# Performance work log

Measured on AMD Instinct MI355X. Metric: run time of the kernel, lower is better.

## Reference

```python
import jax, jax.numpy as jnp
import numpy as np

T, B, D = 1024, 16, 1024
BETA_INIT = 2.0


def _beta_gemm(beta_param, t):
    # beta = sigmoid(raw param); lower-triangular matrix M[i, j] = beta**(i-j) for j <= i
    beta = jax.nn.sigmoid(beta_param)
    i = jnp.arange(t)[:, None]
    j = jnp.arange(t)[None, :]
    expo = i - j                      # [T, T]
    mask = expo >= 0
    # clamp exponent in masked-out region to avoid inf from negative powers
    mat = beta ** jnp.where(mask, expo, 0).astype(beta.dtype)
    return jnp.where(mask, mat, jnp.zeros((), beta.dtype))


def setup_inputs() -> dict:
    key = jax.random.key(0)
    k1, _ = jax.random.split(key)
    x_seq = jax.random.normal(k1, (T, B, D), dtype=jnp.float32)
    beta_param = jnp.asarray(BETA_INIT, dtype=jnp.float32)
    return {"x_seq": x_seq, "beta_param": beta_param}


def reference(x_seq, beta_param):
    t = x_seq.shape[0]
    beta_gemm = _beta_gemm(beta_param, t)            # [T, T] lower-tri decay
    flat = x_seq.reshape(t, -1)                       # [T, B*D]
    y = beta_gemm @ flat                              # addmm with zero bias
    return y.reshape(x_seq.shape)
```

## Files before the change

kernel.cpp:

```cpp
#include <hip/hip_runtime.h>
#include <math.h>

#define T_DIM 1024
#define C_DIM 16384
#define WAVES 16
#define BLOCK_T (WAVES * 64)
#define L_CHUNK (T_DIM / WAVES)

__global__ __launch_bounds__(BLOCK_T, 4)
void pli_scan_kernel(const float* __restrict__ x,
                     const float* __restrict__ beta_p,
                     float* __restrict__ out) {
    const int lane = threadIdx.x & 63;
    const int w    = threadIdx.x >> 6;
    const int col  = (blockIdx.x << 6) + lane;

    const float beta = 1.0f / (1.0f + expf(-beta_p[0]));

    const size_t base = (size_t)(w * L_CHUNK) * C_DIM + col;
    const float* xp = x + base;

    float v[L_CHUNK];
#pragma unroll
    for (int t = 0; t < L_CHUNK; ++t) {
        v[t] = xp[(size_t)t * C_DIM];
    }

    float run = 0.0f;
#pragma unroll
    for (int t = 0; t < L_CHUNK; ++t) {
        run = fmaf(run, beta, v[t]);
        v[t] = run;
    }

    __shared__ float carry[WAVES][64];
    carry[w][lane] = run;
    __syncthreads();

    float bL = beta;
#pragma unroll
    for (int i = 0; i < 6; ++i) bL *= bL;

    float Y = 0.0f;
    for (int u = 0; u < w; ++u) {
        Y = fmaf(Y, bL, carry[u][lane]);
    }

    float m = beta * Y;
    float* op = out + base;
#pragma unroll
    for (int t = 0; t < L_CHUNK; ++t) {
        op[(size_t)t * C_DIM] = v[t] + m;
        m *= beta;
    }
}

extern "C" void kernel_launch(void* const* d_in, const int* in_sizes, int n_in,
                              void* d_out, int out_size, void* d_ws, size_t ws_size,
                              hipStream_t stream) {
    const float* x      = (const float*)d_in[0];
    const float* beta_p = (const float*)d_in[1];
    float* out          = (float*)d_out;

    dim3 grid(C_DIM / 64);
    dim3 block(BLOCK_T);
    hipLaunchKernelGGL(pli_scan_kernel, grid, block, 0, stream, x, beta_p, out);
}
```

Before: 110.4 us.

## Use cooperative grid-sync chunked scan with global carry workspace

Adds a cooperative kernel that splits time into 16 chunks across blocks instead of across waves within one block. Each block does a local scan, writes its chunk carry to a global workspace, syncs the whole grid, then adds the decayed prefix of earlier carries. The aim is wider rows per block for better coalescing and a different work layout. In exchange it adds a grid-wide barrier, global carry traffic and a dependence on cooperative launch support and workspace size. The old kernel remains as a fallback.

```diff
diff --git a/kernel.cpp b/kernel.cpp
--- a/kernel.cpp
+++ b/kernel.cpp
@@ -1,8 +1,67 @@
 #include <hip/hip_runtime.h>
+#include <hip/hip_cooperative_groups.h>
 #include <math.h>
 
 #define T_DIM 1024
 #define C_DIM 16384
+#define TGROUPS 16
+#define CGROUPS 16
+#define TC (T_DIM / TGROUPS)
+#define CC (C_DIM / CGROUPS)
+#define BLOCK_N 1024
+
+namespace cg = cooperative_groups;
+
+__global__ __launch_bounds__(BLOCK_N, 4)
+void pli_scan_coop(const float* __restrict__ x,
+                   const float* __restrict__ beta_p,
+                   float* __restrict__ out,
+                   float* __restrict__ carry) {
+    const int tg  = blockIdx.x >> 4;
+    const int cgi = blockIdx.x & 15;
+    const int col = (cgi << 10) + threadIdx.x;
+
+    const float beta = 1.0f / (1.0f + expf(-beta_p[0]));
+
+    const size_t base = (size_t)(tg * TC) * C_DIM + col;
+    const float* xp = x + base;
+
+    float v[TC];
+#pragma unroll
+    for (int r = 0; r < TC; ++r) {
+        v[r] = xp[(size_t)r * C_DIM];
+    }
+
+    float run = 0.0f;
+#pragma unroll
+    for (int r = 0; r < TC; ++r) {
+        run = fmaf(run, beta, v[r]);
+        v[r] = run;
+    }
+
+    carry[tg * C_DIM + col] = run;
+
+    __threadfence();
+    cg::this_grid().sync();
+
+    float bL = beta;
+#pragma unroll
+    for (int i = 0; i < 6; ++i) bL *= bL;
+
+    float Y = 0.0f;
+    for (int u = 0; u < tg; ++u) {
+        Y = fmaf(Y, bL, carry[u * C_DIM + col]);
+    }
+
+    float m = beta * Y;
+    float* op = out + base;
+#pragma unroll
+    for (int r = 0; r < TC; ++r) {
+        op[(size_t)r * C_DIM] = v[r] + m;
+        m *= beta;
+    }
+}
+
 #define WAVES 16
 #define BLOCK_T (WAVES * 64)
 #define L_CHUNK (T_DIM / WAVES)
@@ -22,19 +81,14 @@
 
     float v[L_CHUNK];
 #pragma unroll
-    for (int t = 0; t < L_CHUNK; ++t) {
-        v[t] = xp[(size_t)t * C_DIM];
-    }
+    for (int t = 0; t < L_CHUNK; ++t) v[t] = xp[(size_t)t * C_DIM];
 
     float run = 0.0f;
 #pragma unroll
-    for (int t = 0; t < L_CHUNK; ++t) {
-        run = fmaf(run, beta, v[t]);
-        v[t] = run;
-    }
+    for (int t = 0; t < L_CHUNK; ++t) { run = fmaf(run, beta, v[t]); v[t] = run; }
 
-    __shared__ float carry[WAVES][64];
-    carry[w][lane] = run;
+    __shared__ float carry_s[WAVES][64];
+    carry_s[w][lane] = run;
     __syncthreads();
 
     float bL = beta;
@@ -42,9 +96,7 @@
     for (int i = 0; i < 6; ++i) bL *= bL;
 
     float Y = 0.0f;
-    for (int u = 0; u < w; ++u) {
-        Y = fmaf(Y, bL, carry[u][lane]);
-    }
+    for (int u = 0; u < w; ++u) Y = fmaf(Y, bL, carry_s[u][lane]);
 
     float m = beta * Y;
     float* op = out + base;
@@ -62,7 +114,19 @@
     const float* beta_p = (const float*)d_in[1];
     float* out          = (float*)d_out;
 
-    dim3 grid(C_DIM / 64);
-    dim3 block(BLOCK_T);
-    hipLaunchKernelGGL(pli_scan_kernel, grid, block, 0, stream, x, beta_p, out);
+    const size_t carry_bytes = (size_t)TGROUPS * C_DIM * sizeof(float);
+
+    if (d_ws != nullptr && ws_size >= carry_bytes) {
+        float* carry = (float*)d_ws;
+        dim3 grid(TGROUPS * CGROUPS);
+        dim3 block(BLOCK_N);
+        void* args[] = { (void*)&x, (void*)&beta_p, (void*)&out, (void*)&carry };
+        hipLaunchCooperativeKernel((const void*)pli_scan_coop, grid, block,
+                                   args, 0, stream);
+    } else {
+        dim3 grid(C_DIM / 64);
+        dim3 block(BLOCK_T);
+        hipLaunchKernelGGL(pli_scan_kernel, grid, block, 0, stream,
+                           x, beta_p, out);
+    }
 }
```

Result: slower. 252.0 us (+128.3%).

## Split scan into carry and apply kernels with float4 loads across time groups

Applied to the files above, without the earlier changes.

Replaces the single-kernel chunked scan with two kernels: one that computes per-time-chunk carries into workspace, and one that folds the preceding carries and rescans each chunk to write the output. Both use float4 vector loads and spread the work over many more blocks (64 time groups × column blocks) to raise parallelism and memory-level concurrency. The cost is reading the input twice plus a second launch and a carry round-trip through global memory. The old kernel stays as a fallback when no workspace is available.

```diff
diff --git a/kernel.cpp b/kernel.cpp
--- a/kernel.cpp
+++ b/kernel.cpp
@@ -3,6 +3,87 @@
 
 #define T_DIM 1024
 #define C_DIM 16384
+#define CQ    (C_DIM / 4)
+#define BLK   256
+
+__device__ __forceinline__ float sigmoid_beta(const float* bp) {
+    return 1.0f / (1.0f + expf(-bp[0]));
+}
+
+template<int TG>
+__global__ __launch_bounds__(BLK)
+void pli_carry(const float* __restrict__ x,
+               const float* __restrict__ beta_p,
+               float* __restrict__ carry) {
+    constexpr int TC = T_DIM / TG;
+    const int nb_c = CQ / BLK;
+    const int tg = blockIdx.x / nb_c;
+    const int q  = (blockIdx.x % nb_c) * BLK + threadIdx.x;
+
+    const float beta = sigmoid_beta(beta_p);
+    const float4* xp = (const float4*)x + (size_t)(tg * TC) * CQ + q;
+
+    float4 run = make_float4(0.f, 0.f, 0.f, 0.f);
+#pragma unroll
+    for (int r = 0; r < TC; ++r) {
+        float4 v = xp[(size_t)r * CQ];
+        run.x = fmaf(run.x, beta, v.x);
+        run.y = fmaf(run.y, beta, v.y);
+        run.z = fmaf(run.z, beta, v.z);
+        run.w = fmaf(run.w, beta, v.w);
+    }
+    ((float4*)carry)[(size_t)tg * CQ + q] = run;
+}
+
+template<int TG>
+__global__ __launch_bounds__(BLK)
+void pli_apply(const float* __restrict__ x,
+               const float* __restrict__ beta_p,
+               const float* __restrict__ carry,
+               float* __restrict__ out) {
+    constexpr int TC = T_DIM / TG;
+    const int nb_c = CQ / BLK;
+    const int tg = blockIdx.x / nb_c;
+    const int q  = (blockIdx.x % nb_c) * BLK + threadIdx.x;
+
+    const float beta = sigmoid_beta(beta_p);
+
+    float bL = beta;
+    for (int i = TC; i > 1; i >>= 1) bL *= bL;
+
+    const float4* cp = (const float4*)carry + q;
+    float4 Y = make_float4(0.f, 0.f, 0.f, 0.f);
+    for (int u = 0; u < tg; ++u) {
+        float4 c = cp[(size_t)u * CQ];
+        Y.x = fmaf(Y.x, bL, c.x);
+        Y.y = fmaf(Y.y, bL, c.y);
+        Y.z = fmaf(Y.z, bL, c.z);
+        Y.w = fmaf(Y.w, bL, c.w);
+    }
+
+    float4 m = make_float4(beta * Y.x, beta * Y.y, beta * Y.z, beta * Y.w);
+
+    const float4* xp = (const float4*)x   + (size_t)(tg * TC) * CQ + q;
+    float4*       op = (float4*)out       + (size_t)(tg * TC) * CQ + q;
+
+    float4 run = make_float4(0.f, 0.f, 0.f, 0.f);
+#pragma unroll
+    for (int r = 0; r < TC; ++r) {
+        float4 v = xp[(size_t)r * CQ];
+        run.x = fmaf(run.x, beta, v.x);
+        run.y = fmaf(run.y, beta, v.y);
+        run.z = fmaf(run.z, beta, v.z);
+        run.w = fmaf(run.w, beta, v.w);
+        float4 o;
+        o.x = run.x + m.x;
+        o.y = run.y + m.y;
+        o.z = run.z + m.z;
+        o.w = run.w + m.w;
+        op[(size_t)r * CQ] = o;
+        m.x *= beta; m.y *= beta; m.z *= beta; m.w *= beta;
+    }
+}
+
 #define WAVES 16
 #define BLOCK_T (WAVES * 64)
 #define L_CHUNK (T_DIM / WAVES)
@@ -22,19 +103,14 @@
 
     float v[L_CHUNK];
 #pragma unroll
-    for (int t = 0; t < L_CHUNK; ++t) {
-        v[t] = xp[(size_t)t * C_DIM];
-    }
+    for (int t = 0; t < L_CHUNK; ++t) v[t] = xp[(size_t)t * C_DIM];
 
     float run = 0.0f;
 #pragma unroll
-    for (int t = 0; t < L_CHUNK; ++t) {
-        run = fmaf(run, beta, v[t]);
-        v[t] = run;
-    }
+    for (int t = 0; t < L_CHUNK; ++t) { run = fmaf(run, beta, v[t]); v[t] = run; }
 
-    __shared__ float carry[WAVES][64];
-    carry[w][lane] = run;
+    __shared__ float carry_s[WAVES][64];
+    carry_s[w][lane] = run;
     __syncthreads();
 
     float bL = beta;
@@ -42,9 +118,7 @@
     for (int i = 0; i < 6; ++i) bL *= bL;
 
     float Y = 0.0f;
-    for (int u = 0; u < w; ++u) {
-        Y = fmaf(Y, bL, carry[u][lane]);
-    }
+    for (int u = 0; u < w; ++u) Y = fmaf(Y, bL, carry_s[u][lane]);
 
     float m = beta * Y;
     float* op = out + base;
@@ -62,7 +136,24 @@
     const float* beta_p = (const float*)d_in[1];
     float* out          = (float*)d_out;
 
-    dim3 grid(C_DIM / 64);
-    dim3 block(BLOCK_T);
-    hipLaunchKernelGGL(pli_scan_kernel, grid, block, 0, stream, x, beta_p, out);
+    const size_t need64 = (size_t)64 * C_DIM * sizeof(float);
+    const size_t need16 = (size_t)16 * C_DIM * sizeof(float);
+
+    if (d_ws != nullptr && ws_size >= need64) {
+        float* carry = (float*)d_ws;
+        dim3 grid(64 * (CQ / BLK));
+        dim3 block(BLK);
+        hipLaunchKernelGGL((pli_carry<64>), grid, block, 0, stream, x, beta_p, carry);
+        hipLaunchKernelGGL((pli_apply<64>), grid, block, 0, stream, x, beta_p, carry, out);
+    } else if (d_ws != nullptr && ws_size >= need16) {
+        float* carry = (float*)d_ws;
+        dim3 grid(16 * (CQ / BLK));
+        dim3 block(BLK);
+        hipLaunchKernelGGL((pli_carry<16>), grid, block, 0, stream, x, beta_p, carry);
+        hipLaunchKernelGGL((pli_apply<16>), grid, block, 0, stream, x, beta_p, carry, out);
+    } else {
+        dim3 grid(C_DIM / 64);
+        dim3 block(BLOCK_T);
+        hipLaunchKernelGGL(pli_scan_kernel, grid, block, 0, stream, x, beta_p, out);
+    }
 }
```

Result: slower. 122.2 us (+10.7%).
